# Kernel tuning notes

Hardware: AMD Instinct MI355X
Metric: run time of the kernel (lower is better)

## Reference

```python
import jax, jax.numpy as jnp
import numpy as np

BATCH, SEQ, DIM = 256, 80, 1024
HEADS = 8
HID = 4 * DIM
EPS = 1e-5


def _ln(x, g, b):
    mu = jnp.mean(x, axis=-1, keepdims=True)
    var = jnp.mean((x - mu) ** 2, axis=-1, keepdims=True)
    return (x - mu) * jax.lax.rsqrt(var + EPS) * g + b


def setup_inputs() -> dict:
    key = jax.random.key(0)
    ks = jax.random.split(key, 8)
    w = lambda k, shape: jax.random.normal(k, shape, dtype=jnp.float32) * 0.02
    return {
        "x": jax.random.normal(ks[0], (BATCH, SEQ, DIM), dtype=jnp.float32),
        "Wq": w(ks[1], (DIM, DIM)),
        "Wk": w(ks[2], (DIM, DIM)),
        "Wv": w(ks[3], (DIM, DIM)),
        "bias_table": w(ks[4], (2 * SEQ - 1, HEADS)),
        "to_out_g": jnp.ones((DIM,), jnp.float32),
        "to_out_b": jnp.zeros((DIM,), jnp.float32),
        "ln1_g": jnp.ones((DIM,), jnp.float32),
        "ln1_b": jnp.zeros((DIM,), jnp.float32),
        "ln2_g": jnp.ones((DIM,), jnp.float32),
        "ln2_b": jnp.zeros((DIM,), jnp.float32),
        "fc1_w": w(ks[5], (DIM, HID)),
        "fc1_b": jnp.zeros((HID,), jnp.float32),
        "fc2_w": w(ks[6], (HID, DIM)),
        "fc2_b": jnp.zeros((DIM,), jnp.float32),
    }


def reference(x, Wq, Wk, Wv, bias_table, to_out_g, to_out_b,
              ln1_g, ln1_b, ln2_g, ln2_b, fc1_w, fc1_b, fc2_w, fc2_b):
    B, S, E = x.shape
    H = HEADS
    D = E // H
    scale = E ** (-0.5)  # NOTE: full emb_size scale, faithful to source

    q = (x @ Wq).reshape(B, S, H, D).transpose(0, 2, 1, 3)  # bhsd
    k = (x @ Wk).reshape(B, S, H, D).transpose(0, 2, 1, 3)
    v = (x @ Wv).reshape(B, S, H, D).transpose(0, 2, 1, 3)

    attn = jnp.einsum('bhqd,bhkd->bhqk', q, k) * scale
    attn = jax.nn.softmax(attn, axis=-1)

    # relative bias added AFTER softmax (non-standard, faithful)
    idx = jnp.arange(S)[:, None] - jnp.arange(S)[None, :] + (S - 1)  # [S,S] in [0,2S-2]
    bias = bias_table[idx].transpose(2, 0, 1)  # (H, S, S)
    attn = attn + bias[None]

    out = jnp.einsum('bhqk,bhkd->bhqd', attn, v)
    out = out.transpose(0, 2, 1, 3).reshape(B, S, E)
    out = _ln(out, to_out_g, to_out_b)  # LayerNorm inside attention (to_out)

    x = _ln(x + out, ln1_g, ln1_b)      # post-norm residual 1
    h = jax.nn.gelu(x @ fc1_w + fc1_b, approximate=False)  # torch nn.GELU exact
    ff = h @ fc2_w + fc2_b
    return _ln(x + ff, ln2_g, ln2_b)    # post-norm residual 2
```

## Files before the change

### kernel.cpp

```cpp
#include <hip/hip_runtime.h>
#include <stdint.h>

#define BATCH 256
#define SEQ   80
#define DIM   1024
#define HEADS 8
#define HDIM  128
#define HID   4096
#define NTOK  (BATCH * SEQ)

typedef unsigned short u16;
using short8_t = __attribute__((ext_vector_type(8))) short;
using f32x4    = __attribute__((ext_vector_type(4))) float;

__device__ __forceinline__ u16 f2bf(float f) {
  unsigned u = __float_as_uint(f);
  u += 0x7fffu + ((u >> 16) & 1u);
  return (u16)(u >> 16);
}
__device__ __forceinline__ float bf2f(u16 u) {
  return __uint_as_float(((unsigned)u) << 16);
}

__device__ __forceinline__ float gelu_exact(float v) {
  return 0.5f * v * (1.0f + erff(v * 0.70710678118654752f));
}

#define GLD16(gp, lp)                                                   \
  __builtin_amdgcn_global_load_lds(                                     \
      (__attribute__((address_space(1))) void*)(void*)(gp),             \
      (__attribute__((address_space(3))) void*)(void*)(lp), 16, 0, 0)

__global__ __launch_bounds__(256) void cast_bf16_kernel(
    const float* __restrict__ in, u16* __restrict__ out, int n4) {
  int i = blockIdx.x * 256 + threadIdx.x;
  int stride = gridDim.x * 256;
  for (; i < n4; i += stride) {
    float4 v = ((const float4*)in)[i];
    uint2 o;
    o.x = (unsigned)f2bf(v.x) | ((unsigned)f2bf(v.y) << 16);
    o.y = (unsigned)f2bf(v.z) | ((unsigned)f2bf(v.w) << 16);
    ((uint2*)out)[i] = o;
  }
}

__global__ __launch_bounds__(256) void transpose_cast_kernel(
    const float* __restrict__ in, u16* __restrict__ out, int R, int C) {
  __shared__ float tile[32][33];
  int c0 = blockIdx.x * 32, r0 = blockIdx.y * 32;
  for (int k = 0; k < 4; k++) {
    int i = threadIdx.y + k * 8;
    tile[i][threadIdx.x] = in[(size_t)(r0 + i) * C + c0 + threadIdx.x];
  }
  __syncthreads();
  for (int k = 0; k < 4; k++) {
    int i = threadIdx.y + k * 8;
    out[(size_t)(c0 + i) * R + r0 + threadIdx.x] = f2bf(tile[threadIdx.x][i]);
  }
}

template <int EPI>
__global__ __launch_bounds__(512, 2) void gemm8s(
    const u16* __restrict__ A, const u16* __restrict__ Bt,
    const float* __restrict__ bias, u16* __restrict__ outp, u16* __restrict__ outp1,
    int M, int N, int Keff, int Ks, int ntn, int ntm) {
  __shared__ __align__(16) u16 lds[65536];

  const int tid = threadIdx.x;
  const int lane = tid & 63, wave = tid >> 6;
  const int wm = wave >> 2, wn = wave & 3;
  const int lo = lane & 15, hi = lane >> 4;

  const int nwg = gridDim.x;
  int q8 = nwg >> 3, r8 = nwg & 7;
  int xcd = blockIdx.x & 7, off = blockIdx.x >> 3;
  int swz = (xcd < r8 ? xcd * (q8 + 1) : r8 * (q8 + 1) + (xcd - r8) * q8) + off;
  const int per = ntn * ntm;
  const int kp = swz / per, rem = swz % per;
  const int bn = rem % ntn, bm = rem / ntn;
  const size_t arow0 = (size_t)bm * 256, bcol0 = (size_t)bn * 256;
  const int kbase = kp * Keff;

  const int srow = tid >> 2;
  const int slb  = (tid & 3) ^ ((srow >> 1) & 3);
  const u16* sA = A + (arow0 + srow) * (size_t)Ks + kbase + slb * 8;
  const u16* sB = Bt + (bcol0 + srow) * (size_t)Ks + kbase + slb * 8;
  const size_t sstep = 128 * (size_t)Ks;

  const int arow = wm * 128 + lo;
  const int brow = wn * 64 + lo;
  const int aoff = arow * 32 + (hi ^ ((arow >> 1) & 3)) * 8;
  const int boff = brow * 32 + (hi ^ ((brow >> 1) & 3)) * 8;

  f32x4 acc[8][4] = {};
  const int NT = Keff >> 6;
  const int NI = NT >> 1;

#define STG(mat, buf, kh, t)                                                  \
  do {                                                                        \
    const u16* s_ = ((mat) ? sB : sA) + (size_t)(t) * 64 + (kh) * 32;         \
    u16* d_ = lds + ((((buf) << 2) | ((mat) << 1) | (kh)) << 13) + wave * 512;\
    GLD16(s_, d_);                                                            \
    GLD16(s_ + sstep, d_ + 4096);                                             \
  } while (0)

#define RD_A(buf, kh, mh, dst)                                                \
  _Pragma("unroll") for (int mi = 0; mi < 4; ++mi)                            \
      dst[mi] = *(const short8_t*)&lds[((((buf) << 2) | (kh)) << 13) + aoff + \
                                       ((mh) * 4 + mi) * 512];

#define RD_B(buf, kh, dst)                                                    \
  _Pragma("unroll") for (int ni = 0; ni < 4; ++ni)                            \
      dst[ni] = *(const short8_t*)&lds[((((buf) << 2) | 2 | (kh)) << 13) +    \
                                       boff + ni * 512];

#define MFMA16(mh, a_, b_)                                                    \
  __builtin_amdgcn_s_setprio(1);                                              \
  _Pragma("unroll") for (int mi = 0; mi < 4; ++mi)                            \
  _Pragma("unroll") for (int ni = 0; ni < 4; ++ni)                            \
      acc[(mh) * 4 + mi][ni] = __builtin_amdgcn_mfma_f32_16x16x32_bf16(       \
          a_[mi], b_[ni], acc[(mh) * 4 + mi][ni], 0, 0, 0);                   \
  __builtin_amdgcn_s_setprio(0);

#define BAR()   asm volatile("s_barrier" ::: "memory")
#define VM(n)   asm volatile("s_waitcnt vmcnt(" #n ")" ::: "memory")

  STG(0, 0, 0, 0); STG(1, 0, 0, 0); STG(0, 0, 1, 0); STG(1, 0, 1, 0);
  STG(0, 1, 0, 1); STG(1, 1, 0, 1); STG(1, 1, 1, 1);
  asm volatile("s_waitcnt vmcnt(0)" ::: "memory");
  BAR();

  short8_t aR0[4], aR1[4], bR0[4], bR1[4];

  for (int i = 0; i < NI - 1; ++i) {
    const int t0 = 2 * i, t1 = 2 * i + 1;
    RD_A(0, 0, 0, aR0); RD_B(0, 0, bR0);
    MFMA16(0, aR0, bR0);
    RD_A(0, 0, 1, aR1);
    STG(0, 1, 1, t1);
    VM(8); BAR();
    MFMA16(1, aR1, bR0);
    RD_A(0, 1, 0, aR0); RD_B(0, 1, bR1);
    STG(1, 0, 0, t0 + 2);
    BAR();
    MFMA16(0, aR0, bR1);
    RD_A(0, 1, 1, aR1);
    STG(0, 0, 0, t0 + 2);
    VM(8); BAR();
    MFMA16(1, aR1, bR1);
    RD_A(1, 0, 0, aR0); RD_B(1, 0, bR0);
    STG(1, 0, 1, t0 + 2);
    BAR();
    MFMA16(0, aR0, bR0);
    RD_A(1, 0, 1, aR1);
    STG(0, 0, 1, t0 + 2);
    VM(8); BAR();
    MFMA16(1, aR1, bR0);
    RD_A(1, 1, 0, aR0); RD_B(1, 1, bR1);
    STG(1, 1, 0, t1 + 2);
    BAR();
    MFMA16(0, aR0, bR1);
    RD_A(1, 1, 1, aR1);
    STG(0, 1, 0, t1 + 2);
    BAR();
    MFMA16(1, aR1, bR1);
    STG(1, 1, 1, t1 + 2);
    VM(10); BAR();
  }

  {
    const int t1 = NT - 1;
    RD_A(0, 0, 0, aR0); RD_B(0, 0, bR0);
    MFMA16(0, aR0, bR0);
    RD_A(0, 0, 1, aR1);
    STG(0, 1, 1, t1);
    VM(8); BAR();
    MFMA16(1, aR1, bR0);
    RD_A(0, 1, 0, aR0); RD_B(0, 1, bR1);
    BAR();
    MFMA16(0, aR0, bR1);
    RD_A(0, 1, 1, aR1);
    VM(4); BAR();
    MFMA16(1, aR1, bR1);
    RD_A(1, 0, 0, aR0); RD_B(1, 0, bR0);
    BAR();
    MFMA16(0, aR0, bR0);
    RD_A(1, 0, 1, aR1);
    VM(0); BAR();
    MFMA16(1, aR1, bR0);
    RD_A(1, 1, 0, aR0); RD_B(1, 1, bR1);
    BAR();
    MFMA16(0, aR0, bR1);
    RD_A(1, 1, 1, aR1);
    BAR();
    MFMA16(1, aR1, bR1);
    BAR();
  }
#undef STG
#undef RD_A
#undef RD_B
#undef MFMA16

  asm volatile("s_waitcnt vmcnt(0)" ::: "memory");
  __syncthreads();

  u16* ct = lds;
#pragma unroll
  for (int n = 0; n < 4; ++n) {
    int col = wn * 64 + n * 16 + lo;
    float bv = 0.f;
    if constexpr (EPI != 0) bv = bias[bcol0 + col];
#pragma unroll
    for (int m = 0; m < 8; ++m) {
#pragma unroll
      for (int j = 0; j < 4; ++j) {
        int row = wm * 128 + m * 16 + hi * 4 + j;
        float v = acc[m][n][j] + bv;
        if constexpr (EPI == 1) v = gelu_exact(v);
        ct[row * 256 + col] = f2bf(v);
      }
    }
  }
  __syncthreads();
  u16* op = (kp ? outp1 : outp) + arow0 * (size_t)N + bcol0;
#pragma unroll
  for (int i = 0; i < 16; ++i) {
    int c = i * 512 + tid;
    int row = c >> 5, o2 = (c & 31) * 8;
    *(short8_t*)(op + (size_t)row * N + o2) = *(const short8_t*)&ct[row * 256 + o2];
  }
}

__global__ __launch_bounds__(64) void attn_kernel(
    const u16* __restrict__ QKV, const float* __restrict__ bias_table,
    u16* __restrict__ attnout) {
  __shared__ __align__(16) u16 Kt[80 * 128];
  __shared__ __align__(16) u16 Vt[96 * 128];
  __shared__ float bias_l[159];

  const int bh = blockIdx.x;
  const int b = bh >> 3, h = bh & 7;
  const int lane = threadIdx.x, lo = lane & 15, hi = lane >> 4;
  const size_t tokbase = (size_t)b * SEQ * 3072;
  const u16* Qg = QKV + tokbase + h * HDIM;
  const u16* Kg = QKV + tokbase + 1024 + h * HDIM;
  const u16* Vg = QKV + tokbase + 2048 + h * HDIM;

#pragma unroll
  for (int i = 0; i < 20; i++) {
    int flat = i * 64 + lane;
    int row = flat >> 4;
    int col = (flat & 15) * 8;
    GLD16(Kg + (size_t)row * 3072 + col, &Kt[i * 512]);
    GLD16(Vg + (size_t)row * 3072 + col, &Vt[i * 512]);
  }
  for (int i = lane; i < 16 * 128; i += 64) Vt[80 * 128 + i] = 0;
  for (int i = lane; i < 159; i += 64) bias_l[i] = bias_table[i * 8 + h];
  asm volatile("s_waitcnt vmcnt(0)" ::: "memory");
  __syncthreads();

  f32x4 sa[5][5] = {};
#pragma unroll
  for (int ks = 0; ks < 4; ks++) {
    short8_t ak[5], bq[5];
#pragma unroll
    for (int m = 0; m < 5; m++)
      ak[m] = *(const short8_t*)&Kt[(m * 16 + lo) * 128 + ks * 32 + hi * 8];
#pragma unroll
    for (int n = 0; n < 5; n++)
      bq[n] = *(const short8_t*)(Qg + (size_t)(n * 16 + lo) * 3072 + ks * 32 + hi * 8);
#pragma unroll
    for (int m = 0; m < 5; m++)
#pragma unroll
      for (int n = 0; n < 5; n++)
        sa[m][n] = __builtin_amdgcn_mfma_f32_16x16x32_bf16(ak[m], bq[n], sa[m][n], 0, 0, 0);
  }
  __syncthreads();

  u16* p_lds = Kt;
  for (int i = lane; i < 80 * 16; i += 64) {
    int q = i >> 4, c = 80 + (i & 15);
    p_lds[q * 104 + c] = 0;
  }
  const float scale = 0.03125f;
#pragma unroll
  for (int n = 0; n < 5; n++) {
    float mx = -1e30f;
#pragma unroll
    for (int m = 0; m < 5; m++)
#pragma unroll
      for (int j = 0; j < 4; j++) {
        sa[m][n][j] *= scale;
        mx = fmaxf(mx, sa[m][n][j]);
      }
    mx = fmaxf(mx, __shfl_xor(mx, 16));
    mx = fmaxf(mx, __shfl_xor(mx, 32));
    float sm = 0.f;
#pragma unroll
    for (int m = 0; m < 5; m++)
#pragma unroll
      for (int j = 0; j < 4; j++) {
        float e = __expf(sa[m][n][j] - mx);
        sa[m][n][j] = e;
        sm += e;
      }
    sm += __shfl_xor(sm, 16);
    sm += __shfl_xor(sm, 32);
    float inv = 1.0f / sm;
    int q = n * 16 + lo;
#pragma unroll
    for (int m = 0; m < 5; m++)
#pragma unroll
      for (int j = 0; j < 4; j++) {
        int key = m * 16 + hi * 4 + j;
        float pv = sa[m][n][j] * inv + bias_l[q - key + 79];
        p_lds[q * 104 + key] = f2bf(pv);
      }
  }
  __syncthreads();

#pragma unroll
  for (int half = 0; half < 2; half++) {
    f32x4 oa[5][4] = {};
#pragma unroll
    for (int ks = 0; ks < 3; ks++) {
      short8_t ap[5];
#pragma unroll
      for (int m = 0; m < 5; m++)
        ap[m] = *(const short8_t*)&p_lds[(m * 16 + lo) * 104 + ks * 32 + hi * 8];
      short8_t bv[4];
#pragma unroll
      for (int nd = 0; nd < 4; nd++) {
        int d = (half * 4 + nd) * 16 + lo;
        short8_t tt;
#pragma unroll
        for (int j = 0; j < 8; j++)
          tt[j] = (short)Vt[(ks * 32 + hi * 8 + j) * 128 + d];
        bv[nd] = tt;
      }
#pragma unroll
      for (int m = 0; m < 5; m++)
#pragma unroll
        for (int nd = 0; nd < 4; nd++)
          oa[m][nd] = __builtin_amdgcn_mfma_f32_16x16x32_bf16(ap[m], bv[nd], oa[m][nd], 0, 0, 0);
    }
#pragma unroll
    for (int m = 0; m < 5; m++)
#pragma unroll
      for (int nd = 0; nd < 4; nd++)
#pragma unroll
        for (int j = 0; j < 4; j++) {
          int q = m * 16 + hi * 4 + j;
          int d = (half * 4 + nd) * 16 + lo;
          attnout[((size_t)b * SEQ + q) * DIM + h * HDIM + d] = f2bf(oa[m][nd][j]);
        }
  }
}

__device__ __forceinline__ void block_reduce2(float& a, float& b, float* sbuf) {
#pragma unroll
  for (int m = 1; m < 64; m <<= 1) {
    a += __shfl_xor(a, m);
    b += __shfl_xor(b, m);
  }
  int w = threadIdx.x >> 6;
  if ((threadIdx.x & 63) == 0) { sbuf[w * 2] = a; sbuf[w * 2 + 1] = b; }
  __syncthreads();
  a = sbuf[0] + sbuf[2] + sbuf[4] + sbuf[6];
  b = sbuf[1] + sbuf[3] + sbuf[5] + sbuf[7];
  __syncthreads();
}

__global__ __launch_bounds__(256) void fuse1_kernel(
    const u16* __restrict__ attnout, const float* __restrict__ x,
    const float* __restrict__ og, const float* __restrict__ ob,
    const float* __restrict__ g1, const float* __restrict__ b1,
    u16* __restrict__ x1b) {
  __shared__ float sbuf[8];
  const size_t base = (size_t)blockIdx.x * DIM;
  float a[4], r[4];
  float s0 = 0.f, s1 = 0.f;
#pragma unroll
  for (int i = 0; i < 4; i++) {
    int idx = threadIdx.x + i * 256;
    a[i] = bf2f(attnout[base + idx]);
    s0 += a[i];
    s1 += a[i] * a[i];
  }
  block_reduce2(s0, s1, sbuf);
  float mu = s0 * (1.f / DIM);
  float rstd = rsqrtf(s1 * (1.f / DIM) - mu * mu + 1e-5f);
  float t0 = 0.f, t1 = 0.f;
#pragma unroll
  for (int i = 0; i < 4; i++) {
    int idx = threadIdx.x + i * 256;
    float o = (a[i] - mu) * rstd * og[idx] + ob[idx];
    r[i] = x[base + idx] + o;
    t0 += r[i];
    t1 += r[i] * r[i];
  }
  block_reduce2(t0, t1, sbuf);
  float mu2 = t0 * (1.f / DIM);
  float rstd2 = rsqrtf(t1 * (1.f / DIM) - mu2 * mu2 + 1e-5f);
#pragma unroll
  for (int i = 0; i < 4; i++) {
    int idx = threadIdx.x + i * 256;
    x1b[base + idx] = f2bf((r[i] - mu2) * rstd2 * g1[idx] + b1[idx]);
  }
}

__global__ __launch_bounds__(256) void fuse2_kernel(
    const u16* __restrict__ x1b, const u16* __restrict__ p0,
    const u16* __restrict__ p1, const float* __restrict__ fc2b,
    const float* __restrict__ g2, const float* __restrict__ b2,
    float* __restrict__ out) {
  __shared__ float sbuf[8];
  const size_t base = (size_t)blockIdx.x * DIM;
  float r[4];
  float s0 = 0.f, s1 = 0.f;
#pragma unroll
  for (int i = 0; i < 4; i++) {
    int idx = threadIdx.x + i * 256;
    r[i] = bf2f(x1b[base + idx]) + bf2f(p0[base + idx]) + bf2f(p1[base + idx]) +
           fc2b[idx];
    s0 += r[i];
    s1 += r[i] * r[i];
  }
  block_reduce2(s0, s1, sbuf);
  float mu = s0 * (1.f / DIM);
  float rstd = rsqrtf(s1 * (1.f / DIM) - mu * mu + 1e-5f);
#pragma unroll
  for (int i = 0; i < 4; i++) {
    int idx = threadIdx.x + i * 256;
    out[base + idx] = (r[i] - mu) * rstd * g2[idx] + b2[idx];
  }
}

extern "C" void kernel_launch(void* const* d_in, const int* in_sizes, int n_in,
                              void* d_out, int out_size, void* d_ws, size_t ws_size,
                              hipStream_t stream) {
  const float* x        = (const float*)d_in[0];
  const float* Wq       = (const float*)d_in[1];
  const float* Wk       = (const float*)d_in[2];
  const float* Wv       = (const float*)d_in[3];
  const float* bias_tab = (const float*)d_in[4];
  const float* og       = (const float*)d_in[5];
  const float* ob       = (const float*)d_in[6];
  const float* g1       = (const float*)d_in[7];
  const float* b1       = (const float*)d_in[8];
  const float* g2       = (const float*)d_in[9];
  const float* b2       = (const float*)d_in[10];
  const float* fc1w     = (const float*)d_in[11];
  const float* fc1b     = (const float*)d_in[12];
  const float* fc2w     = (const float*)d_in[13];
  const float* fc2b     = (const float*)d_in[14];

  char* ws = (char*)d_ws;
  u16* wqkvT = (u16*)(ws + 0);
  u16* fc1T  = (u16*)(ws + 6291456ull);
  u16* fc2T  = (u16*)(ws + 14680064ull);
  u16* pbuf  = (u16*)(ws + 23068672ull);
  u16* qbuf  = (u16*)(ws + 65011712ull);
  char* cbuf = ws + 106954752ull;
  size_t cavail = ws_size > 106954752ull ? ws_size - 106954752ull : 0;

  int cb = 1;
  while (cb < 16 && (size_t)(BATCH / cb) * SEQ * 3072 * 2 > cavail) cb <<= 1;
  int cf = 1;
  while (cf < 16 && (size_t)(NTOK / cf) * (HID + DIM) * 2 > cavail) cf <<= 1;

  dim3 tb(32, 8);
  cast_bf16_kernel<<<2048, 256, 0, stream>>>(x, qbuf, NTOK * DIM / 4);
  transpose_cast_kernel<<<dim3(32, 32), tb, 0, stream>>>(Wq, wqkvT, 1024, 1024);
  transpose_cast_kernel<<<dim3(32, 32), tb, 0, stream>>>(Wk, wqkvT + 1024 * 1024, 1024, 1024);
  transpose_cast_kernel<<<dim3(32, 32), tb, 0, stream>>>(Wv, wqkvT + 2 * 1024 * 1024, 1024, 1024);
  transpose_cast_kernel<<<dim3(128, 32), tb, 0, stream>>>(fc1w, fc1T, 1024, 4096);
  transpose_cast_kernel<<<dim3(32, 128), tb, 0, stream>>>(fc2w, fc2T, 4096, 1024);

  {
    const int nb = BATCH / cb;
    const int rows = nb * SEQ;
    u16* qkvc = (u16*)cbuf;
    const int ntm = rows / 256;
    const int nwg = ntm * 12;
    for (int c = 0; c < cb; ++c) {
      const u16* xb_c = qbuf + (size_t)c * rows * DIM;
      gemm8s<0><<<nwg, 512, 0, stream>>>(xb_c, wqkvT, nullptr, qkvc, qkvc,
                                         rows, 3072, 1024, 1024, 12, ntm);
      attn_kernel<<<nb * HEADS, 64, 0, stream>>>(
          qkvc, bias_tab, pbuf + (size_t)c * rows * DIM);
    }
  }

  fuse1_kernel<<<NTOK, 256, 0, stream>>>(pbuf, x, og, ob, g1, b1, qbuf);

  {
    const int rows = NTOK / cf;
    u16* hc  = (u16*)cbuf;
    u16* p1c = (u16*)(cbuf + (size_t)rows * HID * 2);
    const int ntm = rows / 256;
    for (int c = 0; c < cf; ++c) {
      const size_t off = (size_t)c * rows * DIM;
      gemm8s<1><<<ntm * 16, 512, 0, stream>>>(qbuf + off, fc1T, fc1b, hc, hc,
                                              rows, HID, 1024, 1024, 16, ntm);
      gemm8s<0><<<ntm * 4 * 2, 512, 0, stream>>>(hc, fc2T, nullptr,
                                                 pbuf + off, p1c,
                                                 rows, 1024, 2048, 4096, 4, ntm);
      fuse2_kernel<<<rows, 256, 0, stream>>>(qbuf + off, pbuf + off, p1c, fc2b,
                                             g2, b2, (float*)d_out + off);
    }
  }
}
```

Before: 747.7 us.

## Switch GEMM to 4-wave 256-thread blocks with 128x128 per-wave tiles

Restructures the 256x256-tile bf16 GEMM from 8 waves (each 128x64) to 4 waves (each 128x128), doubling accumulators per wave and issuing four global-to-LDS loads per staging step instead of two. The aim is more MFMA work per LDS fragment read, fewer waves contending for barriers, and higher arithmetic intensity per wave. In exchange it uses far more VGPRs/AGPRs (256 accumulator floats per lane), allows only one block per CU, and leaves fewer waves to hide latency. The waitcnt thresholds were rescaled to match the extra loads.

```diff
diff --git a/kernel.cpp b/kernel.cpp
--- a/kernel.cpp
+++ b/kernel.cpp
@@ -60,7 +60,7 @@
 }
 
 template <int EPI>
-__global__ __launch_bounds__(512, 2) void gemm8s(
+__global__ __launch_bounds__(256, 1) void gemm4w(
     const u16* __restrict__ A, const u16* __restrict__ Bt,
     const float* __restrict__ bias, u16* __restrict__ outp, u16* __restrict__ outp1,
     int M, int N, int Keff, int Ks, int ntn, int ntm) {
@@ -68,7 +68,7 @@
 
   const int tid = threadIdx.x;
   const int lane = tid & 63, wave = tid >> 6;
-  const int wm = wave >> 2, wn = wave & 3;
+  const int wm = wave >> 1, wn = wave & 1;
   const int lo = lane & 15, hi = lane >> 4;
 
   const int nwg = gridDim.x;
@@ -85,14 +85,14 @@
   const int slb  = (tid & 3) ^ ((srow >> 1) & 3);
   const u16* sA = A + (arow0 + srow) * (size_t)Ks + kbase + slb * 8;
   const u16* sB = Bt + (bcol0 + srow) * (size_t)Ks + kbase + slb * 8;
-  const size_t sstep = 128 * (size_t)Ks;
+  const size_t cstep = 64 * (size_t)Ks;
 
   const int arow = wm * 128 + lo;
-  const int brow = wn * 64 + lo;
+  const int brow = wn * 128 + lo;
   const int aoff = arow * 32 + (hi ^ ((arow >> 1) & 3)) * 8;
   const int boff = brow * 32 + (hi ^ ((brow >> 1) & 3)) * 8;
 
-  f32x4 acc[8][4] = {};
+  f32x4 acc[8][8] = {};
   const int NT = Keff >> 6;
   const int NI = NT >> 1;
 
@@ -101,25 +101,27 @@
     const u16* s_ = ((mat) ? sB : sA) + (size_t)(t) * 64 + (kh) * 32;         \
     u16* d_ = lds + ((((buf) << 2) | ((mat) << 1) | (kh)) << 13) + wave * 512;\
     GLD16(s_, d_);                                                            \
-    GLD16(s_ + sstep, d_ + 4096);                                             \
+    GLD16(s_ + cstep, d_ + 2048);                                             \
+    GLD16(s_ + 2 * cstep, d_ + 4096);                                         \
+    GLD16(s_ + 3 * cstep, d_ + 6144);                                         \
   } while (0)
 
-#define RD_A(buf, kh, mh, dst)                                                \
-  _Pragma("unroll") for (int mi = 0; mi < 4; ++mi)                            \
+#define RD_A(buf, kh, dst)                                                    \
+  _Pragma("unroll") for (int mi = 0; mi < 8; ++mi)                            \
       dst[mi] = *(const short8_t*)&lds[((((buf) << 2) | (kh)) << 13) + aoff + \
-                                       ((mh) * 4 + mi) * 512];
-
-#define RD_B(buf, kh, dst)                                                    \
+                                       mi * 512];
+
+#define RD_B(buf, kh, nh, dst)                                                \
   _Pragma("unroll") for (int ni = 0; ni < 4; ++ni)                            \
       dst[ni] = *(const short8_t*)&lds[((((buf) << 2) | 2 | (kh)) << 13) +    \
-                                       boff + ni * 512];
-
-#define MFMA16(mh, a_, b_)                                                    \
+                                       boff + ((nh) * 4 + ni) * 512];
+
+#define MFMAP(a_, b_, nh)                                                     \
   __builtin_amdgcn_s_setprio(1);                                              \
-  _Pragma("unroll") for (int mi = 0; mi < 4; ++mi)                            \
+  _Pragma("unroll") for (int mi = 0; mi < 8; ++mi)                            \
   _Pragma("unroll") for (int ni = 0; ni < 4; ++ni)                            \
-      acc[(mh) * 4 + mi][ni] = __builtin_amdgcn_mfma_f32_16x16x32_bf16(       \
-          a_[mi], b_[ni], acc[(mh) * 4 + mi][ni], 0, 0, 0);                   \
+      acc[mi][(nh) * 4 + ni] = __builtin_amdgcn_mfma_f32_16x16x32_bf16(       \
+          a_[mi], b_[ni], acc[mi][(nh) * 4 + ni], 0, 0, 0);                   \
   __builtin_amdgcn_s_setprio(0);
 
 #define BAR()   asm volatile("s_barrier" ::: "memory")
@@ -130,84 +132,84 @@
   asm volatile("s_waitcnt vmcnt(0)" ::: "memory");
   BAR();
 
-  short8_t aR0[4], aR1[4], bR0[4], bR1[4];
+  short8_t A0[8], A1[8], B0[4], B1[4];
 
   for (int i = 0; i < NI - 1; ++i) {
     const int t0 = 2 * i, t1 = 2 * i + 1;
-    RD_A(0, 0, 0, aR0); RD_B(0, 0, bR0);
-    MFMA16(0, aR0, bR0);
-    RD_A(0, 0, 1, aR1);
+    RD_A(0, 0, A0); RD_B(0, 0, 0, B0);
+    MFMAP(A0, B0, 0);
+    RD_B(0, 0, 1, B1);
     STG(0, 1, 1, t1);
-    VM(8); BAR();
-    MFMA16(1, aR1, bR0);
-    RD_A(0, 1, 0, aR0); RD_B(0, 1, bR1);
+    VM(16); BAR();
+    MFMAP(A0, B1, 1);
+    RD_A(0, 1, A1); RD_B(0, 1, 0, B0);
     STG(1, 0, 0, t0 + 2);
     BAR();
-    MFMA16(0, aR0, bR1);
-    RD_A(0, 1, 1, aR1);
+    MFMAP(A1, B0, 0);
+    RD_B(0, 1, 1, B1);
     STG(0, 0, 0, t0 + 2);
-    VM(8); BAR();
-    MFMA16(1, aR1, bR1);
-    RD_A(1, 0, 0, aR0); RD_B(1, 0, bR0);
+    VM(16); BAR();
+    MFMAP(A1, B1, 1);
+    RD_A(1, 0, A0); RD_B(1, 0, 0, B0);
     STG(1, 0, 1, t0 + 2);
     BAR();
-    MFMA16(0, aR0, bR0);
-    RD_A(1, 0, 1, aR1);
+    MFMAP(A0, B0, 0);
+    RD_B(1, 0, 1, B1);
     STG(0, 0, 1, t0 + 2);
-    VM(8); BAR();
-    MFMA16(1, aR1, bR0);
-    RD_A(1, 1, 0, aR0); RD_B(1, 1, bR1);
+    VM(16); BAR();
+    MFMAP(A0, B1, 1);
+    RD_A(1, 1, A1); RD_B(1, 1, 0, B0);
     STG(1, 1, 0, t1 + 2);
     BAR();
-    MFMA16(0, aR0, bR1);
-    RD_A(1, 1, 1, aR1);
+    MFMAP(A1, B0, 0);
+    RD_B(1, 1, 1, B1);
     STG(0, 1, 0, t1 + 2);
     BAR();
-    MFMA16(1, aR1, bR1);
+    MFMAP(A1, B1, 1);
     STG(1, 1, 1, t1 + 2);
-    VM(10); BAR();
+    VM(20); BAR();
   }
 
   {
     const int t1 = NT - 1;
-    RD_A(0, 0, 0, aR0); RD_B(0, 0, bR0);
-    MFMA16(0, aR0, bR0);
-    RD_A(0, 0, 1, aR1);
+    RD_A(0, 0, A0); RD_B(0, 0, 0, B0);
+    MFMAP(A0, B0, 0);
+    RD_B(0, 0, 1, B1);
     STG(0, 1, 1, t1);
+    VM(16); BAR();
+    MFMAP(A0, B1, 1);
+    RD_A(0, 1, A1); RD_B(0, 1, 0, B0);
+    BAR();
+    MFMAP(A1, B0, 0);
+    RD_B(0, 1, 1, B1);
     VM(8); BAR();
-    MFMA16(1, aR1, bR0);
-    RD_A(0, 1, 0, aR0); RD_B(0, 1, bR1);
-    BAR();
-    MFMA16(0, aR0, bR1);
-    RD_A(0, 1, 1, aR1);
-    VM(4); BAR();
-    MFMA16(1, aR1, bR1);
-    RD_A(1, 0, 0, aR0); RD_B(1, 0, bR0);
-    BAR();
-    MFMA16(0, aR0, bR0);
-    RD_A(1, 0, 1, aR1);
+    MFMAP(A1, B1, 1);
+    RD_A(1, 0, A0); RD_B(1, 0, 0, B0);
+    BAR();
+    MFMAP(A0, B0, 0);
+    RD_B(1, 0, 1, B1);
     VM(0); BAR();
-    MFMA16(1, aR1, bR0);
-    RD_A(1, 1, 0, aR0); RD_B(1, 1, bR1);
-    BAR();
-    MFMA16(0, aR0, bR1);
-    RD_A(1, 1, 1, aR1);
-    BAR();
-    MFMA16(1, aR1, bR1);
+    MFMAP(A0, B1, 1);
+    RD_A(1, 1, A1); RD_B(1, 1, 0, B0);
+    BAR();
+    MFMAP(A1, B0, 0);
+    RD_B(1, 1, 1, B1);
+    BAR();
+    MFMAP(A1, B1, 1);
     BAR();
   }
 #undef STG
 #undef RD_A
 #undef RD_B
-#undef MFMA16
+#undef MFMAP
 
   asm volatile("s_waitcnt vmcnt(0)" ::: "memory");
   __syncthreads();
 
   u16* ct = lds;
 #pragma unroll
-  for (int n = 0; n < 4; ++n) {
-    int col = wn * 64 + n * 16 + lo;
+  for (int n = 0; n < 8; ++n) {
+    int col = wn * 128 + n * 16 + lo;
     float bv = 0.f;
     if constexpr (EPI != 0) bv = bias[bcol0 + col];
 #pragma unroll
@@ -224,8 +226,8 @@
   __syncthreads();
   u16* op = (kp ? outp1 : outp) + arow0 * (size_t)N + bcol0;
 #pragma unroll
-  for (int i = 0; i < 16; ++i) {
-    int c = i * 512 + tid;
+  for (int i = 0; i < 32; ++i) {
+    int c = i * 256 + tid;
     int row = c >> 5, o2 = (c & 31) * 8;
     *(short8_t*)(op + (size_t)row * N + o2) = *(const short8_t*)&ct[row * 256 + o2];
   }
@@ -485,7 +487,7 @@
     const int nwg = ntm * 12;
     for (int c = 0; c < cb; ++c) {
       const u16* xb_c = qbuf + (size_t)c * rows * DIM;
-      gemm8s<0><<<nwg, 512, 0, stream>>>(xb_c, wqkvT, nullptr, qkvc, qkvc,
+      gemm4w<0><<<nwg, 256, 0, stream>>>(xb_c, wqkvT, nullptr, qkvc, qkvc,
                                          rows, 3072, 1024, 1024, 12, ntm);
       attn_kernel<<<nb * HEADS, 64, 0, stream>>>(
           qkvc, bias_tab, pbuf + (size_t)c * rows * DIM);
@@ -501,9 +503,9 @@
     const int ntm = rows / 256;
     for (int c = 0; c < cf; ++c) {
       const size_t off = (size_t)c * rows * DIM;
-      gemm8s<1><<<ntm * 16, 512, 0, stream>>>(qbuf + off, fc1T, fc1b, hc, hc,
+      gemm4w<1><<<ntm * 16, 256, 0, stream>>>(qbuf + off, fc1T, fc1b, hc, hc,
                                               rows, HID, 1024, 1024, 16, ntm);
-      gemm8s<0><<<ntm * 4 * 2, 512, 0, stream>>>(hc, fc2T, nullptr,
+      gemm4w<0><<<ntm * 4 * 2, 256, 0, stream>>>(hc, fc2T, nullptr,
                                                  pbuf + off, p1c,
                                                  rows, 1024, 2048, 4096, 4, ntm);
       fuse2_kernel<<<rows, 256, 0, stream>>>(qbuf + off, pbuf + off, p1c, fc2b,
```

Measured after the change: 919.6 us. 1.23x slower.
